# Kernel tuning notes

Hardware: AMD Instinct MI355X
Metric: run time of the kernel (lower is better)

The kernel has to match this reference:

```python
import jax, jax.numpy as jnp
import numpy as np

HEADS = 4  # from init_kwargs

def _branch_index(seq_len: int) -> jnp.ndarray:
    # position 0 -> layer_s(0), 1 -> layer_r(1), 2 -> layer_o(2),
    # then alternating layer_a(3)/layer_v(4) starting at position 3.
    tail = jnp.where((jnp.arange(seq_len - 3) % 2) == 0, 3, 4)
    return jnp.concatenate([jnp.array([0, 1, 2], dtype=tail.dtype), tail])


def setup_inputs() -> dict:
    key = jax.random.key(0)
    k1, k2, k3 = jax.random.split(key, 3)
    B, S, H = 128, 513, 256
    x = jax.random.normal(k1, (B, S, H), dtype=jnp.float32)
    # 5 Linear layers, nn.Linear convention: y = x @ W.T + b, W: [out,in]
    W = jax.random.normal(k2, (5, H, H), dtype=jnp.float32) * (1.0 / np.sqrt(H))
    b = jax.random.normal(k3, (5, H), dtype=jnp.float32) * 0.02
    return {"x": x, "W": W, "b": b}


def reference(x, W, b):
    # Original applies each Linear to a position-masked copy of x and sums.
    # Since the 5 masks are disjoint one-hots over positions, the weight term
    # at position t is x[t] @ W[m(t)].T; the bias term is sum of ALL 5 biases
    # (Linear(0) = bias), applied at every position.
    B, S, H = x.shape
    idx = _branch_index(S)            # [S] in {0..4}
    Wsel = W[idx]
    out = jnp.einsum('bsh,sdh->bsd', x, Wsel) + b.sum(axis=0)
    return out.reshape(B, S, HEADS, H // HEADS)
```

## Files before the change

kernel.cpp:

```cpp
#include <hip/hip_runtime.h>
#include <hip/hip_bf16.h>

#define B_ 128
#define S_ 513
#define H_ 256

typedef __attribute__((ext_vector_type(8))) short short8;
typedef __attribute__((ext_vector_type(4))) float f32x4;

static __device__ inline short8 pack8(float4 a, float4 b) {
    union { short8 s; __hip_bfloat162 h[4]; } u;
    u.h[0] = __float22bfloat162_rn(make_float2(a.x, a.y));
    u.h[1] = __float22bfloat162_rn(make_float2(a.z, a.w));
    u.h[2] = __float22bfloat162_rn(make_float2(b.x, b.y));
    u.h[3] = __float22bfloat162_rn(make_float2(b.z, b.w));
    return u.s;
}

static __device__ inline unsigned short f2bf(float f) {
    union { float f; unsigned int u; } v; v.f = f;
    unsigned int u = v.u;
    unsigned int r = u + 0x7fffu + ((u >> 16) & 1u);
    return (unsigned short)(r >> 16);
}

__global__ __launch_bounds__(256, 3)
void sel_gemm_kernel(const float* __restrict__ x,
                     const float* __restrict__ W,
                     const float* __restrict__ bias,
                     float* __restrict__ out) {
    const int bx = blockIdx.x;
    const int s  = bx >> 1;
    const int h  = bx & 1;
    const int m_idx = (s < 3) ? s : ((s & 1) ? 3 : 4);

    __shared__ unsigned short As[64 * 264];

    const int t    = threadIdx.x;
    const int lane = t & 63;
    const int w    = t >> 6;
    const int lrow = lane & 15;
    const int quad = lane >> 4;

    const float* xbase = x + ((size_t)(h * 64) * S_ + s) * H_;
    const float* Wbase = W + (size_t)m_idx * H_ * H_;

#pragma unroll
    for (int i = 0; i < 16; ++i) {
        int flat = i * 256 + t;
        int row  = flat >> 6;
        int col  = (flat & 63) * 4;
        const float4 v = *(const float4*)(xbase + (size_t)row * (S_ * H_) + col);
        ushort4 p;
        p.x = f2bf(v.x); p.y = f2bf(v.y); p.z = f2bf(v.z); p.w = f2bf(v.w);
        *(ushort4*)&As[row * 264 + col] = p;
    }

    f32x4 acc[4][4];
#pragma unroll
    for (int i = 0; i < 4; ++i)
#pragma unroll
        for (int j = 0; j < 4; ++j) {
            f32x4 z = {0.f, 0.f, 0.f, 0.f};
            acc[i][j] = z;
        }

    const float* Wrow[4];
#pragma unroll
    for (int j = 0; j < 4; ++j)
        Wrow[j] = Wbase + (size_t)(w * 64 + j * 16 + lrow) * H_;

    __syncthreads();

#pragma unroll 2
    for (int kk = 0; kk < 8; ++kk) {
        const int kf = kk * 32 + quad * 8;
        short8 a_frag[4];
#pragma unroll
        for (int i = 0; i < 4; ++i)
            a_frag[i] = *(const short8*)&As[(i * 16 + lrow) * 264 + kf];
#pragma unroll
        for (int j = 0; j < 4; ++j) {
            const float4 w0 = *(const float4*)(Wrow[j] + kf);
            const float4 w1 = *(const float4*)(Wrow[j] + kf + 4);
            const short8 b_frag = pack8(w0, w1);
#pragma unroll
            for (int i = 0; i < 4; ++i)
                acc[i][j] = __builtin_amdgcn_mfma_f32_16x16x32_bf16(
                    a_frag[i], b_frag, acc[i][j], 0, 0, 0);
        }
    }

    float bsum[4];
#pragma unroll
    for (int j = 0; j < 4; ++j) {
        int d = w * 64 + j * 16 + lrow;
        float sum = 0.f;
#pragma unroll
        for (int i = 0; i < 5; ++i) sum += bias[i * H_ + d];
        bsum[j] = sum;
    }

#pragma unroll
    for (int i = 0; i < 4; ++i) {
#pragma unroll
        for (int r = 0; r < 4; ++r) {
            int bg = h * 64 + i * 16 + quad * 4 + r;
            float* orow = out + ((size_t)bg * S_ + s) * H_;
#pragma unroll
            for (int j = 0; j < 4; ++j) {
                int d = w * 64 + j * 16 + lrow;
                orow[d] = acc[i][j][r] + bsum[j];
            }
        }
    }
}

extern "C" void kernel_launch(void* const* d_in, const int* in_sizes, int n_in,
                              void* d_out, int out_size, void* d_ws, size_t ws_size,
                              hipStream_t stream) {
    const float* x    = (const float*)d_in[0];
    const float* W    = (const float*)d_in[1];
    const float* bias = (const float*)d_in[2];
    float* out = (float*)d_out;

    dim3 grid(S_ * 2);
    dim3 block(256);
    sel_gemm_kernel<<<grid, block, 0, stream>>>(x, W, bias, out);
}
```

Baseline: 154.5 us.

## Merge batch halves into one block per position, preconvert W to bf16

Each block now covers all 128 batch rows of a position with 512 threads, so the selected weight matrix is loaded once per position instead of twice. A prep kernel converts the five weight matrices to bf16 and presums the biases into workspace. The main kernel keeps its weight fragments entirely in registers and uses an XOR-swizzled LDS layout for the activation tile in place of padding. In exchange it adds a second launch and heavy register pressure (32 short8 fragments per thread), and halves the grid to 513 blocks.

New measurement: 137.2 us. 1.13x faster.

```diff
diff --git a/kernel.cpp b/kernel.cpp
--- a/kernel.cpp
+++ b/kernel.cpp
@@ -4,6 +4,7 @@
 #define B_ 128
 #define S_ 513
 #define H_ 256
+#define SH_ (S_ * H_)
 
 typedef __attribute__((ext_vector_type(8))) short short8;
 typedef __attribute__((ext_vector_type(4))) float f32x4;
@@ -24,36 +25,79 @@
     return (unsigned short)(r >> 16);
 }
 
-__global__ __launch_bounds__(256, 3)
+__global__ void prep_kernel(const float* __restrict__ W,
+                            const float* __restrict__ bias,
+                            unsigned short* __restrict__ Wbf,
+                            float* __restrict__ bsum) {
+    int t = blockIdx.x * 256 + threadIdx.x;
+    if (t < 5 * H_ * H_ / 4) {
+        float4 v = *(const float4*)(W + (size_t)t * 4);
+        ushort4 p;
+        p.x = f2bf(v.x); p.y = f2bf(v.y); p.z = f2bf(v.z); p.w = f2bf(v.w);
+        *(ushort4*)(Wbf + (size_t)t * 4) = p;
+    }
+    if (t < H_) {
+        float s = 0.f;
+#pragma unroll
+        for (int i = 0; i < 5; ++i) s += bias[i * H_ + t];
+        bsum[t] = s;
+    }
+}
+
+template <int MODE>
+__global__ __launch_bounds__(512, 2)
 void sel_gemm_kernel(const float* __restrict__ x,
-                     const float* __restrict__ W,
-                     const float* __restrict__ bias,
+                     const void* __restrict__ Wp,
+                     const void* __restrict__ bp,
                      float* __restrict__ out) {
-    const int bx = blockIdx.x;
-    const int s  = bx >> 1;
-    const int h  = bx & 1;
+    const int s = blockIdx.x;
     const int m_idx = (s < 3) ? s : ((s & 1) ? 3 : 4);
 
-    __shared__ unsigned short As[64 * 264];
+    __shared__ unsigned short As[128 * 256];
 
     const int t    = threadIdx.x;
     const int lane = t & 63;
     const int w    = t >> 6;
+    const int wn   = w & 3;
+    const int wm   = w >> 1 >> 1;
     const int lrow = lane & 15;
     const int quad = lane >> 4;
 
-    const float* xbase = x + ((size_t)(h * 64) * S_ + s) * H_;
-    const float* Wbase = W + (size_t)m_idx * H_ * H_;
+    short8 bfr[4][8];
+    if (MODE == 0) {
+        const unsigned short* Wb =
+            (const unsigned short*)Wp + (size_t)m_idx * H_ * H_;
+#pragma unroll
+        for (int j = 0; j < 4; ++j) {
+            const unsigned short* wrow = Wb + (size_t)(wn * 64 + j * 16 + lrow) * H_;
+#pragma unroll
+            for (int kk = 0; kk < 8; ++kk)
+                bfr[j][kk] = *(const short8*)(wrow + kk * 32 + quad * 8);
+        }
+    } else {
+        const float* Wb = (const float*)Wp + (size_t)m_idx * H_ * H_;
+#pragma unroll
+        for (int j = 0; j < 4; ++j) {
+            const float* wrow = Wb + (size_t)(wn * 64 + j * 16 + lrow) * H_;
+#pragma unroll
+            for (int kk = 0; kk < 8; ++kk) {
+                float4 v0 = *(const float4*)(wrow + kk * 32 + quad * 8);
+                float4 v1 = *(const float4*)(wrow + kk * 32 + quad * 8 + 4);
+                bfr[j][kk] = pack8(v0, v1);
+            }
+        }
+    }
 
+    const float* xs = x + (size_t)s * H_;
 #pragma unroll
-    for (int i = 0; i < 16; ++i) {
-        int flat = i * 256 + t;
-        int row  = flat >> 6;
-        int col  = (flat & 63) * 4;
-        const float4 v = *(const float4*)(xbase + (size_t)row * (S_ * H_) + col);
-        ushort4 p;
-        p.x = f2bf(v.x); p.y = f2bf(v.y); p.z = f2bf(v.z); p.w = f2bf(v.w);
-        *(ushort4*)&As[row * 264 + col] = p;
+    for (int i = 0; i < 8; ++i) {
+        int flat = i * 512 + t;
+        int r = flat >> 5;
+        int c = flat & 31;
+        const float* src = xs + (size_t)r * SH_ + c * 8;
+        float4 v0 = *(const float4*)src;
+        float4 v1 = *(const float4*)(src + 4);
+        *(short8*)&As[r * 256 + ((c ^ (r & 7)) * 8)] = pack8(v0, v1);
     }
 
     f32x4 acc[4][4];
@@ -65,52 +109,52 @@
             acc[i][j] = z;
         }
 
-    const float* Wrow[4];
-#pragma unroll
-    for (int j = 0; j < 4; ++j)
-        Wrow[j] = Wbase + (size_t)(w * 64 + j * 16 + lrow) * H_;
-
     __syncthreads();
 
-#pragma unroll 2
+#pragma unroll
     for (int kk = 0; kk < 8; ++kk) {
-        const int kf = kk * 32 + quad * 8;
-        short8 a_frag[4];
+        const int cc = kk * 4 + quad;
+        short8 afr[4];
 #pragma unroll
-        for (int i = 0; i < 4; ++i)
-            a_frag[i] = *(const short8*)&As[(i * 16 + lrow) * 264 + kf];
+        for (int i = 0; i < 4; ++i) {
+            int r = wm * 64 + i * 16 + lrow;
+            afr[i] = *(const short8*)&As[r * 256 + ((cc ^ (r & 7)) * 8)];
+        }
 #pragma unroll
-        for (int j = 0; j < 4; ++j) {
-            const float4 w0 = *(const float4*)(Wrow[j] + kf);
-            const float4 w1 = *(const float4*)(Wrow[j] + kf + 4);
-            const short8 b_frag = pack8(w0, w1);
+        for (int j = 0; j < 4; ++j)
 #pragma unroll
             for (int i = 0; i < 4; ++i)
                 acc[i][j] = __builtin_amdgcn_mfma_f32_16x16x32_bf16(
-                    a_frag[i], b_frag, acc[i][j], 0, 0, 0);
-        }
+                    afr[i], bfr[j][kk], acc[i][j], 0, 0, 0);
     }
 
-    float bsum[4];
+    float bs[4];
+    if (MODE == 0) {
+        const float* bsum = (const float*)bp;
 #pragma unroll
-    for (int j = 0; j < 4; ++j) {
-        int d = w * 64 + j * 16 + lrow;
-        float sum = 0.f;
+        for (int j = 0; j < 4; ++j) bs[j] = bsum[wn * 64 + j * 16 + lrow];
+    } else {
+        const float* bias = (const float*)bp;
 #pragma unroll
-        for (int i = 0; i < 5; ++i) sum += bias[i * H_ + d];
-        bsum[j] = sum;
+        for (int j = 0; j < 4; ++j) {
+            int d = wn * 64 + j * 16 + lrow;
+            float sum = 0.f;
+#pragma unroll
+            for (int i = 0; i < 5; ++i) sum += bias[i * H_ + d];
+            bs[j] = sum;
+        }
     }
 
 #pragma unroll
     for (int i = 0; i < 4; ++i) {
 #pragma unroll
         for (int r = 0; r < 4; ++r) {
-            int bg = h * 64 + i * 16 + quad * 4 + r;
+            int bg = wm * 64 + i * 16 + quad * 4 + r;
             float* orow = out + ((size_t)bg * S_ + s) * H_;
 #pragma unroll
             for (int j = 0; j < 4; ++j) {
-                int d = w * 64 + j * 16 + lrow;
-                orow[d] = acc[i][j][r] + bsum[j];
+                int d = wn * 64 + j * 16 + lrow;
+                orow[d] = acc[i][j][r] + bs[j];
             }
         }
     }
@@ -124,7 +168,18 @@
     const float* bias = (const float*)d_in[2];
     float* out = (float*)d_out;
 
-    dim3 grid(S_ * 2);
-    dim3 block(256);
-    sel_gemm_kernel<<<grid, block, 0, stream>>>(x, W, bias, out);
+    const size_t w_elems  = (size_t)5 * H_ * H_;
+    const size_t ws_need  = w_elems * sizeof(unsigned short) + H_ * sizeof(float);
+
+    if (ws_size >= ws_need) {
+        unsigned short* Wbf = (unsigned short*)d_ws;
+        float* bsum = (float*)((char*)d_ws + w_elems * sizeof(unsigned short));
+        prep_kernel<<<dim3((w_elems / 4 + 255) / 256), dim3(256), 0, stream>>>(
+            W, bias, Wbf, bsum);
+        sel_gemm_kernel<0><<<dim3(S_), dim3(512), 0, stream>>>(
+            x, (const void*)Wbf, (const void*)bsum, out);
+    } else {
+        sel_gemm_kernel<1><<<dim3(S_), dim3(512), 0, stream>>>(
+            x, (const void*)W, (const void*)bias, out);
+    }
 }
```
